# Optimization experiments

Measured on AMD Instinct MI355X. Metric: run time of the kernel, lower is better.

The kernel has to match this reference:

```python
import jax, jax.numpy as jnp
import numpy as np

N = 100000   # nodes
E = 800000   # edges
F_IN = 128   # in_channels
C = 64       # out_channels
H = 2 * C    # hidden = 2*out_channels


def _w(key, shape, fan_in):
    return jax.random.normal(key, shape, jnp.float32) * (1.0 / np.sqrt(fan_in))


def setup_inputs() -> dict:
    key = jax.random.key(0)
    ks = jax.random.split(key, 12)
    return {
        "x": jax.random.normal(ks[0], (N, F_IN), jnp.float32),
        "edge_index": jax.random.randint(ks[1], (2, E), 0, N, dtype=jnp.int32),
        # layer 1 (F_IN -> H)
        "W1_in": _w(ks[2], (F_IN, H), F_IN),
        "W1_out": _w(ks[3], (F_IN, H), F_IN),
        "W1_root": _w(ks[4], (F_IN, H), F_IN),
        "b1": jnp.zeros((H,), jnp.float32),
        # layer 2 (H -> C)
        "W2_in": _w(ks[5], (H, C), H),
        "W2_out": _w(ks[6], (H, C), H),
        "W2_root": _w(ks[7], (H, C), H),
        "b2": jnp.zeros((C,), jnp.float32),
    }


def _gcn(x, W, src, dst):
    # GCNConv with add_self_loops=False, bias=None:
    # out[dst] += deg^-1/2[src] * deg^-1/2[dst] * (x @ W)[src]
    h = x @ W
    deg = jax.ops.segment_sum(jnp.ones_like(dst, jnp.float32), dst, num_segments=N)
    dinv = jnp.where(deg > 0, jax.lax.rsqrt(jnp.maximum(deg, 1.0)), 0.0)
    norm = dinv[src] * dinv[dst]                 # [E]
    msg = h[src] * norm[:, None]                 # [E, F_out]
    return jax.ops.segment_sum(msg, dst, num_segments=N)


def _dir_layer(x, W_in, W_out, W_root, b, src, dst, alpha=0.5):
    x_in = _gcn(x, W_in, src, dst)               # original direction
    x_out = _gcn(x, W_out, dst, src)             # flipped edges
    return alpha * x_out + (1.0 - alpha) * x_in + x @ W_root + b


def reference(x, edge_index, W1_in, W1_out, W1_root, b1, W2_in, W2_out, W2_root, b2):
    src, dst = edge_index[0], edge_index[1]
    h = jax.nn.relu(_dir_layer(x, W1_in, W1_out, W1_root, b1, src, dst))
    return _dir_layer(h, W2_in, W2_out, W2_root, b2, src, dst)
```

## Files before the change

kernel.cpp:

```cpp
#include <hip/hip_runtime.h>

typedef __attribute__((ext_vector_type(8))) short bf16x8;
typedef __attribute__((ext_vector_type(4))) float f32x4;

#define NB 196
#define CAP 8192
#define SBLK 256
#define ECH 3125

__device__ __forceinline__ unsigned short f2bf(float f) {
    unsigned int u = __float_as_uint(f);
    u = (u + 0x7FFFu + ((u >> 16) & 1u)) >> 16;
    return (unsigned short)u;
}
__device__ __forceinline__ float bf2f(unsigned short v) {
    return __uint_as_float(((unsigned int)v) << 16);
}

template<int BNW, bool A_FP32>
__global__ __launch_bounds__(256)
void gemm3_k(const void* __restrict__ Av,
             const unsigned short* __restrict__ BTcat,
             const float* __restrict__ bias,
             const float* __restrict__ dinv_in, const float* __restrict__ dinv_out,
             unsigned short* __restrict__ Y0, unsigned short* __restrict__ Y1,
             unsigned short* __restrict__ Y2, int nrows)
{
    constexpr int CF = BNW / 32;
    __shared__ unsigned short As[64 * 128];
    __shared__ unsigned short Bs[BNW * 128];

    const int t  = threadIdx.x;
    const int w  = t >> 6, l = t & 63;
    const int g  = l >> 4, li = l & 15;
    const int wr = w >> 1, wc = w & 1;
    const int row0 = blockIdx.x * 64;

    if (A_FP32) {
        const float* Ag = (const float*)Av;
        #pragma unroll
        for (int i = 0; i < 4; ++i) {
            const int q   = t + 256 * i;
            const int row = q >> 4;
            const int ck  = q & 15;
            unsigned short o[8];
            if (row0 + row < nrows) {
                const float* src = Ag + (size_t)(row0 + row) * 128 + ck * 8;
                const float4 a = *(const float4*)src;
                const float4 b = *(const float4*)(src + 4);
                o[0]=f2bf(a.x); o[1]=f2bf(a.y); o[2]=f2bf(a.z); o[3]=f2bf(a.w);
                o[4]=f2bf(b.x); o[5]=f2bf(b.y); o[6]=f2bf(b.z); o[7]=f2bf(b.w);
            } else {
                #pragma unroll
                for (int u = 0; u < 8; ++u) o[u] = 0;
            }
            *(int4*)&As[row * 128 + ((ck ^ (row & 7)) << 3)] = *(int4*)o;
        }
    } else {
        const int4* Ag = (const int4*)((const unsigned short*)Av + (size_t)row0 * 128);
        #pragma unroll
        for (int i = 0; i < 4; ++i) {
            const int q   = t + 256 * i;
            const int row = q >> 4;
            const int ck  = q & 15;
            const int4 v  = Ag[q];
            *(int4*)&As[row * 128 + ((ck ^ (row & 7)) << 3)] = v;
        }
    }

    #pragma unroll 1
    for (int wgt = 0; wgt < 3; ++wgt) {
        __syncthreads();
        {
            const int4* Bg = (const int4*)(BTcat + (size_t)wgt * BNW * 128);
            #pragma unroll
            for (int i = 0; i < BNW / 16; ++i) {
                const int q   = t + 256 * i;
                const int row = q >> 4;
                const int ck  = q & 15;
                const int4 v  = Bg[q];
                *(int4*)&Bs[row * 128 + ((ck ^ (row & 7)) << 3)] = v;
            }
        }
        __syncthreads();

        f32x4 acc[2][CF];
        #pragma unroll
        for (int rf = 0; rf < 2; ++rf)
            #pragma unroll
            for (int cf = 0; cf < CF; ++cf)
                acc[rf][cf] = (f32x4){0.f, 0.f, 0.f, 0.f};

        #pragma unroll
        for (int kk = 0; kk < 4; ++kk) {
            bf16x8 av[2], bv[CF];
            #pragma unroll
            for (int rf = 0; rf < 2; ++rf) {
                const int ar = wr * 32 + rf * 16 + li;
                const int ck = (kk * 4 + g) ^ (ar & 7);
                av[rf] = *(const bf16x8*)&As[ar * 128 + (ck << 3)];
            }
            #pragma unroll
            for (int cf = 0; cf < CF; ++cf) {
                const int bc = wc * (BNW / 2) + cf * 16 + li;
                const int ck = (kk * 4 + g) ^ (bc & 7);
                bv[cf] = *(const bf16x8*)&Bs[bc * 128 + (ck << 3)];
            }
            #pragma unroll
            for (int rf = 0; rf < 2; ++rf)
                #pragma unroll
                for (int cf = 0; cf < CF; ++cf)
                    acc[rf][cf] = __builtin_amdgcn_mfma_f32_16x16x32_bf16(
                        av[rf], bv[cf], acc[rf][cf], 0, 0, 0);
        }

        unsigned short* Y = (wgt == 0) ? Y0 : (wgt == 1) ? Y1 : Y2;
        const float* dv = (wgt == 1) ? dinv_in : dinv_out;
        #pragma unroll
        for (int rf = 0; rf < 2; ++rf) {
            #pragma unroll
            for (int i = 0; i < 4; ++i) {
                const int r = row0 + wr * 32 + rf * 16 + 4 * g + i;
                if (r < nrows) {
                    const float s = (wgt == 0) ? 1.f : 0.5f * dv[r];
                    #pragma unroll
                    for (int cf = 0; cf < CF; ++cf) {
                        const int c = wc * (BNW / 2) + cf * 16 + li;
                        float v = acc[rf][cf][i];
                        v = (wgt == 0) ? (v + bias[c]) : (v * s);
                        Y[(size_t)r * BNW + c] = f2bf(v);
                    }
                }
            }
        }
    }
}

__global__ __launch_bounds__(256)
void wtrans_all_k(const float* __restrict__ W1r, const float* __restrict__ W1i,
                  const float* __restrict__ W1o, const float* __restrict__ W2r,
                  const float* __restrict__ W2i, const float* __restrict__ W2o,
                  unsigned short* __restrict__ T1, unsigned short* __restrict__ T2)
{
    const int tid = blockIdx.x * 256 + threadIdx.x;
    if (tid >= 3 * 16384 + 3 * 8192) return;
    const float* W; unsigned short* T; int M, r, base;
    if (tid < 49152) {
        const int w = tid / 16384; r = tid % 16384; M = 128;
        W = (w == 0) ? W1r : (w == 1) ? W1i : W1o;
        T = T1; base = w * 128;
    } else {
        const int u = tid - 49152;
        const int w = u / 8192; r = u % 8192; M = 64;
        W = (w == 0) ? W2r : (w == 1) ? W2i : W2o;
        T = T2; base = w * 64;
    }
    const int m = r & (M - 1);
    const int k = r / M;
    T[(size_t)(base + m) * 128 + k] = f2bf(W[(size_t)k * M + m]);
}

__global__ __launch_bounds__(256)
void zero_i_k(int* __restrict__ p, int n)
{
    const int i = blockIdx.x * 256 + threadIdx.x;
    if (i < n) p[i] = 0;
}

__global__ __launch_bounds__(256)
void bscatter_k(const int* __restrict__ src, const int* __restrict__ dst,
                int* __restrict__ bcnt_in, int* __restrict__ bcnt_out,
                int* __restrict__ ebuf_in, int* __restrict__ ebuf_out, int E)
{
    __shared__ int lcnt_d[NB], lcnt_s[NB], lbase_d[NB], lbase_s[NB];
    const int t = threadIdx.x;
    const int c0 = blockIdx.x * ECH;
    const int c1 = min(E, c0 + ECH);
    for (int i = t; i < NB; i += 256) { lcnt_d[i] = 0; lcnt_s[i] = 0; }
    __syncthreads();
    for (int e = c0 + t; e < c1; e += 256) {
        atomicAdd(&lcnt_d[dst[e] >> 9], 1);
        atomicAdd(&lcnt_s[src[e] >> 9], 1);
    }
    __syncthreads();
    for (int b = t; b < NB; b += 256) {
        lbase_d[b] = atomicAdd(&bcnt_in[b],  lcnt_d[b]);
        lbase_s[b] = atomicAdd(&bcnt_out[b], lcnt_s[b]);
        lcnt_d[b] = 0; lcnt_s[b] = 0;
    }
    __syncthreads();
    for (int e = c0 + t; e < c1; e += 256) {
        const int s = src[e], d = dst[e];
        const int bd = d >> 9, bs = s >> 9;
        const int rd = atomicAdd(&lcnt_d[bd], 1);
        ebuf_in [bd * CAP + lbase_d[bd] + rd] = (s << 9) | (d & 511);
        const int rs = atomicAdd(&lcnt_s[bs], 1);
        ebuf_out[bs * CAP + lbase_s[bs] + rs] = (d << 9) | (s & 511);
    }
}

__global__ __launch_bounds__(256)
void bscan_k(const int* __restrict__ bcnt_in, const int* __restrict__ bcnt_out,
             int* __restrict__ bsc_in, int* __restrict__ bsc_out)
{
    __shared__ int s[256];
    const int t = threadIdx.x;
    for (int pass = 0; pass < 2; ++pass) {
        const int* c = pass ? bcnt_out : bcnt_in;
        int* o = pass ? bsc_out : bsc_in;
        const int v = (t < NB) ? c[t] : 0;
        s[t] = v;
        __syncthreads();
        #pragma unroll
        for (int off = 1; off < 256; off <<= 1) {
            const int tv = (t >= off) ? s[t - off] : 0;
            __syncthreads();
            s[t] += tv;
            __syncthreads();
        }
        if (t < NB) o[t] = s[t] - v;
        if (t == NB - 1) o[NB] = s[t];
        __syncthreads();
    }
}

__global__ __launch_bounds__(512)
void bdegfill_k(const int* __restrict__ ebuf_in, const int* __restrict__ ebuf_out,
                const int* __restrict__ bcnt_in, const int* __restrict__ bcnt_out,
                const int* __restrict__ bsc_in, const int* __restrict__ bsc_out,
                float* __restrict__ dinv_in, float* __restrict__ dinv_out,
                int* __restrict__ rp_in, int* __restrict__ rp_out,
                int* __restrict__ col_in, int* __restrict__ col_out, int N, int E)
{
    __shared__ int cnt[512];
    __shared__ int cur[512];
    const int t = threadIdx.x;
    const int dir = (blockIdx.x >= NB) ? 1 : 0;
    const int b = blockIdx.x - dir * NB;
    const int* ebuf = dir ? ebuf_out : ebuf_in;
    const int ne = (dir ? bcnt_out : bcnt_in)[b];
    const int base = (dir ? bsc_out : bsc_in)[b];
    const int e0 = b * CAP;

    cnt[t] = 0;
    __syncthreads();
    for (int j = t; j < ne; j += 512) atomicAdd(&cnt[ebuf[e0 + j] & 511], 1);
    __syncthreads();

    const int node = b * 512 + t;
    const int deg = cnt[t];
    float* dinv = dir ? dinv_out : dinv_in;
    if (node < N) dinv[node] = (deg > 0) ? rsqrtf((float)deg) : 0.f;

    #pragma unroll
    for (int off = 1; off < 512; off <<= 1) {
        const int tv = (t >= off) ? cnt[t - off] : 0;
        __syncthreads();
        cnt[t] += tv;
        __syncthreads();
    }
    int* rp = dir ? rp_out : rp_in;
    if (node < N) rp[node] = base + cnt[t] - deg;
    if (b == 0 && t == 0) rp[N] = E;
    cur[t] = cnt[t] - deg;
    __syncthreads();

    int* col = dir ? col_out : col_in;
    for (int j = t; j < ne; j += 512) {
        const int p = ebuf[e0 + j];
        const int slot = atomicAdd(&cur[p & 511], 1);
        col[base + slot] = p >> 9;
    }
}

__device__ __forceinline__ void accum8(float* acc, const int4 v) {
    const unsigned short* pp = (const unsigned short*)&v;
    #pragma unroll
    for (int u = 0; u < 8; ++u) acc[u] += bf2f(pp[u]);
}

template<int F, bool RELU_BF16>
__global__ __launch_bounds__(256)
void gather2_k(const unsigned short* __restrict__ h_in,
               const unsigned short* __restrict__ h_out,
               const int* __restrict__ rp_in,  const int* __restrict__ col_in,
               const int* __restrict__ rp_out, const int* __restrict__ col_out,
               const float* __restrict__ dinv_in, const float* __restrict__ dinv_out,
               const unsigned short* __restrict__ ybase, void* __restrict__ yout, int N)
{
    constexpr int TPN = F / 8;
    const int tid = blockIdx.x * 256 + threadIdx.x;
    const int n = tid / TPN;
    if (n >= N) return;
    const int c8 = (tid % TPN) * 8;

    const int bi = rp_in[n],  ei = rp_in[n + 1];
    const int bo = rp_out[n], eo = rp_out[n + 1];
    const float di = dinv_in[n], dq = dinv_out[n];
    const int4 yb4 = *(const int4*)(ybase + (size_t)n * F + c8);

    const unsigned short* hi = h_in + c8;
    const unsigned short* ho = h_out + c8;

    float acc_i[8] = {}, acc_o[8] = {};

    #pragma unroll 1
    for (int pass = 0; pass < 2; ++pass) {
        const int beg = pass ? bo : bi;
        const int end = pass ? eo : ei;
        const int* col = pass ? col_out : col_in;
        const unsigned short* h = pass ? ho : hi;
        float* acc = pass ? acc_o : acc_i;

        int j = beg;
        if (j + 4 <= end) {
            int c0 = col[j], c1 = col[j + 1], c2 = col[j + 2], c3 = col[j + 3];
            for (; j + 8 <= end; j += 4) {
                const int4 v0 = *(const int4*)(h + (size_t)c0 * F);
                const int4 v1 = *(const int4*)(h + (size_t)c1 * F);
                const int4 v2 = *(const int4*)(h + (size_t)c2 * F);
                const int4 v3 = *(const int4*)(h + (size_t)c3 * F);
                c0 = col[j + 4]; c1 = col[j + 5]; c2 = col[j + 6]; c3 = col[j + 7];
                accum8(acc, v0); accum8(acc, v1); accum8(acc, v2); accum8(acc, v3);
            }
            const int4 v0 = *(const int4*)(h + (size_t)c0 * F);
            const int4 v1 = *(const int4*)(h + (size_t)c1 * F);
            const int4 v2 = *(const int4*)(h + (size_t)c2 * F);
            const int4 v3 = *(const int4*)(h + (size_t)c3 * F);
            accum8(acc, v0); accum8(acc, v1); accum8(acc, v2); accum8(acc, v3);
            j += 4;
        }
        if (j < end) {
            const int rem = end - j;
            const int c0 = col[j];
            const int c1 = (rem > 1) ? col[j + 1] : c0;
            const int c2 = (rem > 2) ? col[j + 2] : c0;
            const int4 v0 = *(const int4*)(h + (size_t)c0 * F);
            if (rem > 1) {
                const int4 v1 = *(const int4*)(h + (size_t)c1 * F);
                accum8(acc, v1);
            }
            if (rem > 2) {
                const int4 v2 = *(const int4*)(h + (size_t)c2 * F);
                accum8(acc, v2);
            }
            accum8(acc, v0);
        }
    }

    const unsigned short* yb = (const unsigned short*)&yb4;
    float v[8];
    #pragma unroll
    for (int u = 0; u < 8; ++u)
        v[u] = bf2f(yb[u]) + di * acc_i[u] + dq * acc_o[u];

    if (RELU_BF16) {
        unsigned short o[8];
        #pragma unroll
        for (int u = 0; u < 8; ++u) o[u] = f2bf(fmaxf(v[u], 0.f));
        *(int4*)((unsigned short*)yout + (size_t)n * F + c8) = *(int4*)o;
    } else {
        float* yp = (float*)yout + (size_t)n * F + c8;
        *(float4*)yp       = make_float4(v[0], v[1], v[2], v[3]);
        *(float4*)(yp + 4) = make_float4(v[4], v[5], v[6], v[7]);
    }
}

extern "C" void kernel_launch(void* const* d_in, const int* in_sizes, int n_in,
                              void* d_out, int out_size, void* d_ws, size_t ws_size,
                              hipStream_t stream)
{
    const int N = 100000, E = 800000, C = 64, H = 128;
    const int Npad = ((N + 63) / 64) * 64;

    const float* x       = (const float*)d_in[0];
    const int*   ei      = (const int*)d_in[1];
    const int*   src     = ei;
    const int*   dst     = ei + E;
    const float* W1_in   = (const float*)d_in[2];
    const float* W1_out  = (const float*)d_in[3];
    const float* W1_root = (const float*)d_in[4];
    const float* b1      = (const float*)d_in[5];
    const float* W2_in   = (const float*)d_in[6];
    const float* W2_out  = (const float*)d_in[7];
    const float* W2_root = (const float*)d_in[8];
    const float* b2      = (const float*)d_in[9];
    float* out = (float*)d_out;

    char* p = (char*)d_ws;
    int*   bcnt_in  = (int*)p;            p += (size_t)(2 * NB + 8) * 4;
    int*   bcnt_out = bcnt_in + NB;
    int*   bsc_in   = (int*)p;            p += (size_t)(2 * (NB + 1) + 8) * 4;
    int*   bsc_out  = bsc_in + NB + 1;
    float* dinv_in  = (float*)p;          p += (size_t)N * 4;
    float* dinv_out = (float*)p;          p += (size_t)N * 4;
    int*   rp_in    = (int*)p;            p += (size_t)(N + 8) * 4;
    int*   rp_out   = (int*)p;            p += (size_t)(N + 8) * 4;
    int*   col_in   = (int*)p;            p += (size_t)E * 4;
    int*   col_out  = (int*)p;            p += (size_t)E * 4;
    int*   ebuf_in  = (int*)p;            p += (size_t)NB * CAP * 4;
    int*   ebuf_out = (int*)p;            p += (size_t)NB * CAP * 4;
    unsigned short* wt1 = (unsigned short*)p;       p += (size_t)384 * 128 * 2;
    unsigned short* wt2 = (unsigned short*)p;       p += (size_t)192 * 128 * 2;
    unsigned short* xb  = (unsigned short*)p;       p += (size_t)Npad * 128 * 2;
    unsigned short* y1b = (unsigned short*)p;       p += (size_t)Npad * 128 * 2;
    unsigned short* h_in = (unsigned short*)p;      p += (size_t)Npad * 128 * 2;
    unsigned short* h_out= (unsigned short*)p;      p += (size_t)Npad * 128 * 2;

    const dim3 blk(256);

    zero_i_k<<<(2 * NB + 255) / 256, blk, 0, stream>>>(bcnt_in, 2 * NB);
    bscatter_k<<<SBLK, blk, 0, stream>>>(src, dst, bcnt_in, bcnt_out,
                                         ebuf_in, ebuf_out, E);
    bscan_k<<<1, blk, 0, stream>>>(bcnt_in, bcnt_out, bsc_in, bsc_out);
    bdegfill_k<<<2 * NB, 512, 0, stream>>>(ebuf_in, ebuf_out, bcnt_in, bcnt_out,
                                           bsc_in, bsc_out, dinv_in, dinv_out,
                                           rp_in, rp_out, col_in, col_out, N, E);

    wtrans_all_k<<<288, blk, 0, stream>>>(W1_root, W1_in, W1_out, W2_root, W2_in, W2_out,
                                          wt1, wt2);

    const int gemm_blocks = Npad / 64;
    const int ga1 = (N * (H / 8) + 255) / 256;
    const int ga2 = (N * (C / 8) + 255) / 256;

    gemm3_k<128, true><<<gemm_blocks, blk, 0, stream>>>(
        x, wt1, b1, dinv_in, dinv_out, y1b, h_in, h_out, N);
    gather2_k<128, true><<<ga1, blk, 0, stream>>>(
        h_in, h_out, rp_in, col_in, rp_out, col_out,
        dinv_in, dinv_out, y1b, xb, N);

    gemm3_k<64, false><<<gemm_blocks, blk, 0, stream>>>(
        xb, wt2, b2, dinv_in, dinv_out, y1b, h_in, h_out, N);
    gather2_k<64, false><<<ga2, blk, 0, stream>>>(
        h_in, h_out, rp_in, col_in, rp_out, col_out,
        dinv_in, dinv_out, y1b, out, N);
}
```

Baseline: 269.1 us.

## Store intermediate features in column slabs so gathers hit a smaller cache footprint

The GEMM outputs and the layer-1 activations are now stored in 8 column slabs laid out node-major within each slab. The gather kernel is re-indexed so consecutive blocks handle one slab at a time, which makes each gather pass touch a working set about an eighth the size of the full feature matrix and so stay resident in L2/LLC. The trade-off is that each neighbor's column list and row pointers are re-read once per slab, and each random gather load is now only 16 bytes, which is less efficient per transaction. The second GEMM's A-load and the first gather's output use the same slab layout, so the two stay consistent.

```diff
diff --git a/kernel.cpp b/kernel.cpp
--- a/kernel.cpp
+++ b/kernel.cpp
@@ -17,16 +17,17 @@
     return __uint_as_float(((unsigned int)v) << 16);
 }
 
-template<int BNW, bool A_FP32>
+template<int BNW, int AMODE>
 __global__ __launch_bounds__(256)
 void gemm3_k(const void* __restrict__ Av,
              const unsigned short* __restrict__ BTcat,
              const float* __restrict__ bias,
              const float* __restrict__ dinv_in, const float* __restrict__ dinv_out,
              unsigned short* __restrict__ Y0, unsigned short* __restrict__ Y1,
-             unsigned short* __restrict__ Y2, int nrows)
+             unsigned short* __restrict__ Y2, int nrows, int Npad)
 {
     constexpr int CF = BNW / 32;
+    constexpr int OSLAB = BNW / 8;
     __shared__ unsigned short As[64 * 128];
     __shared__ unsigned short Bs[BNW * 128];
 
@@ -36,7 +37,7 @@
     const int wr = w >> 1, wc = w & 1;
     const int row0 = blockIdx.x * 64;
 
-    if (A_FP32) {
+    if (AMODE == 0) {
         const float* Ag = (const float*)Av;
         #pragma unroll
         for (int i = 0; i < 4; ++i) {
@@ -57,13 +58,14 @@
             *(int4*)&As[row * 128 + ((ck ^ (row & 7)) << 3)] = *(int4*)o;
         }
     } else {
-        const int4* Ag = (const int4*)((const unsigned short*)Av + (size_t)row0 * 128);
+        const unsigned short* Axb = (const unsigned short*)Av;
         #pragma unroll
         for (int i = 0; i < 4; ++i) {
             const int q   = t + 256 * i;
             const int row = q >> 4;
             const int ck  = q & 15;
-            const int4 v  = Ag[q];
+            const size_t addr = ((size_t)(ck >> 1) * Npad + (row0 + row)) * 16 + (ck & 1) * 8;
+            const int4 v = *(const int4*)(Axb + addr);
             *(int4*)&As[row * 128 + ((ck ^ (row & 7)) << 3)] = v;
         }
     }
@@ -128,7 +130,7 @@
                         const int c = wc * (BNW / 2) + cf * 16 + li;
                         float v = acc[rf][cf][i];
                         v = (wgt == 0) ? (v + bias[c]) : (v * s);
-                        Y[(size_t)r * BNW + c] = f2bf(v);
+                        Y[((size_t)(c / OSLAB) * Npad + r) * OSLAB + (c % OSLAB)] = f2bf(v);
                     }
                 }
             }
@@ -281,33 +283,37 @@
 
 template<int F, bool RELU_BF16>
 __global__ __launch_bounds__(256)
-void gather2_k(const unsigned short* __restrict__ h_in,
+void gathers_k(const unsigned short* __restrict__ h_in,
                const unsigned short* __restrict__ h_out,
                const int* __restrict__ rp_in,  const int* __restrict__ col_in,
                const int* __restrict__ rp_out, const int* __restrict__ col_out,
                const float* __restrict__ dinv_in, const float* __restrict__ dinv_out,
-               const unsigned short* __restrict__ ybase, void* __restrict__ yout, int N)
-{
-    constexpr int TPN = F / 8;
-    const int tid = blockIdx.x * 256 + threadIdx.x;
-    const int n = tid / TPN;
+               const unsigned short* __restrict__ ybase, void* __restrict__ yout,
+               int N, int Npad)
+{
+    constexpr int SLAB = F / 8;
+    constexpr int TPN  = SLAB / 8;
+    constexpr int NPB  = 256 / TPN;
+    const int slab = blockIdx.x & 7;
+    const int t = threadIdx.x;
+    const int n = (blockIdx.x >> 3) * NPB + t / TPN;
     if (n >= N) return;
-    const int c8 = (tid % TPN) * 8;
-
-    const int bi = rp_in[n],  ei = rp_in[n + 1];
-    const int bo = rp_out[n], eo = rp_out[n + 1];
+    const int co = (t % TPN) * 8;
+
+    const size_t sbase = (size_t)slab * Npad * SLAB + co;
+    const unsigned short* hi = h_in  + sbase;
+    const unsigned short* ho = h_out + sbase;
+
+    const int bi = rp_in[n],  ei2 = rp_in[n + 1];
+    const int bo = rp_out[n], eo  = rp_out[n + 1];
     const float di = dinv_in[n], dq = dinv_out[n];
-    const int4 yb4 = *(const int4*)(ybase + (size_t)n * F + c8);
-
-    const unsigned short* hi = h_in + c8;
-    const unsigned short* ho = h_out + c8;
 
     float acc_i[8] = {}, acc_o[8] = {};
 
     #pragma unroll 1
     for (int pass = 0; pass < 2; ++pass) {
         const int beg = pass ? bo : bi;
-        const int end = pass ? eo : ei;
+        const int end = pass ? eo : ei2;
         const int* col = pass ? col_out : col_in;
         const unsigned short* h = pass ? ho : hi;
         float* acc = pass ? acc_o : acc_i;
@@ -316,17 +322,17 @@
         if (j + 4 <= end) {
             int c0 = col[j], c1 = col[j + 1], c2 = col[j + 2], c3 = col[j + 3];
             for (; j + 8 <= end; j += 4) {
-                const int4 v0 = *(const int4*)(h + (size_t)c0 * F);
-                const int4 v1 = *(const int4*)(h + (size_t)c1 * F);
-                const int4 v2 = *(const int4*)(h + (size_t)c2 * F);
-                const int4 v3 = *(const int4*)(h + (size_t)c3 * F);
+                const int4 v0 = *(const int4*)(h + (size_t)c0 * SLAB);
+                const int4 v1 = *(const int4*)(h + (size_t)c1 * SLAB);
+                const int4 v2 = *(const int4*)(h + (size_t)c2 * SLAB);
+                const int4 v3 = *(const int4*)(h + (size_t)c3 * SLAB);
                 c0 = col[j + 4]; c1 = col[j + 5]; c2 = col[j + 6]; c3 = col[j + 7];
                 accum8(acc, v0); accum8(acc, v1); accum8(acc, v2); accum8(acc, v3);
             }
-            const int4 v0 = *(const int4*)(h + (size_t)c0 * F);
-            const int4 v1 = *(const int4*)(h + (size_t)c1 * F);
-            const int4 v2 = *(const int4*)(h + (size_t)c2 * F);
-            const int4 v3 = *(const int4*)(h + (size_t)c3 * F);
+            const int4 v0 = *(const int4*)(h + (size_t)c0 * SLAB);
+            const int4 v1 = *(const int4*)(h + (size_t)c1 * SLAB);
+            const int4 v2 = *(const int4*)(h + (size_t)c2 * SLAB);
+            const int4 v3 = *(const int4*)(h + (size_t)c3 * SLAB);
             accum8(acc, v0); accum8(acc, v1); accum8(acc, v2); accum8(acc, v3);
             j += 4;
         }
@@ -335,19 +341,20 @@
             const int c0 = col[j];
             const int c1 = (rem > 1) ? col[j + 1] : c0;
             const int c2 = (rem > 2) ? col[j + 2] : c0;
-            const int4 v0 = *(const int4*)(h + (size_t)c0 * F);
+            const int4 v0 = *(const int4*)(h + (size_t)c0 * SLAB);
             if (rem > 1) {
-                const int4 v1 = *(const int4*)(h + (size_t)c1 * F);
+                const int4 v1 = *(const int4*)(h + (size_t)c1 * SLAB);
                 accum8(acc, v1);
             }
             if (rem > 2) {
-                const int4 v2 = *(const int4*)(h + (size_t)c2 * F);
+                const int4 v2 = *(const int4*)(h + (size_t)c2 * SLAB);
                 accum8(acc, v2);
             }
             accum8(acc, v0);
         }
     }
 
+    const int4 yb4 = *(const int4*)(ybase + sbase + (size_t)n * SLAB);
     const unsigned short* yb = (const unsigned short*)&yb4;
     float v[8];
     #pragma unroll
@@ -358,9 +365,9 @@
         unsigned short o[8];
         #pragma unroll
         for (int u = 0; u < 8; ++u) o[u] = f2bf(fmaxf(v[u], 0.f));
-        *(int4*)((unsigned short*)yout + (size_t)n * F + c8) = *(int4*)o;
+        *(int4*)((unsigned short*)yout + sbase + (size_t)n * SLAB) = *(int4*)o;
     } else {
-        float* yp = (float*)yout + (size_t)n * F + c8;
+        float* yp = (float*)yout + (size_t)n * F + slab * SLAB + co;
         *(float4*)yp       = make_float4(v[0], v[1], v[2], v[3]);
         *(float4*)(yp + 4) = make_float4(v[4], v[5], v[6], v[7]);
     }
@@ -421,18 +428,18 @@
                                           wt1, wt2);
 
     const int gemm_blocks = Npad / 64;
-    const int ga1 = (N * (H / 8) + 255) / 256;
-    const int ga2 = (N * (C / 8) + 255) / 256;
-
-    gemm3_k<128, true><<<gemm_blocks, blk, 0, stream>>>(
-        x, wt1, b1, dinv_in, dinv_out, y1b, h_in, h_out, N);
-    gather2_k<128, true><<<ga1, blk, 0, stream>>>(
+    const int g1 = 8 * ((N + 127) / 128);
+    const int g2 = 8 * ((N + 255) / 256);
+
+    gemm3_k<128, 0><<<gemm_blocks, blk, 0, stream>>>(
+        x, wt1, b1, dinv_in, dinv_out, y1b, h_in, h_out, N, Npad);
+    gathers_k<128, true><<<g1, blk, 0, stream>>>(
         h_in, h_out, rp_in, col_in, rp_out, col_out,
-        dinv_in, dinv_out, y1b, xb, N);
-
-    gemm3_k<64, false><<<gemm_blocks, blk, 0, stream>>>(
-        xb, wt2, b2, dinv_in, dinv_out, y1b, h_in, h_out, N);
-    gather2_k<64, false><<<ga2, blk, 0, stream>>>(
+        dinv_in, dinv_out, y1b, xb, N, Npad);
+
+    gemm3_k<64, 1><<<gemm_blocks, blk, 0, stream>>>(
+        xb, wt2, b2, dinv_in, dinv_out, y1b, h_in, h_out, N, Npad);
+    gathers_k<64, false><<<g2, blk, 0, stream>>>(
         h_in, h_out, rp_in, col_in, rp_out, col_out,
-        dinv_in, dinv_out, y1b, out, N);
-}
+        dinv_in, dinv_out, y1b, out, N, Npad);
+}
```

After: 354.8 us. +31.9%, slower.
